# Optimization experiments

Hardware: AMD Instinct MI355X
Metric: run time of the kernel (lower is better)

Reference implementation:

```python
import jax, jax.numpy as jnp
import numpy as np

N, E, E_LBL = 50000, 800000, 200000
D_IN, H = 128, 128


def setup_inputs() -> dict:
    key = jax.random.key(0)
    ks = jax.random.split(key, 12)
    s = 0.05
    return {
        "x": jax.random.normal(ks[0], (N, D_IN), jnp.float32),
        "edge_index": jax.random.randint(ks[1], (2, E), 0, N, jnp.int64),
        "edge_label_index": jax.random.randint(ks[2], (2, E_LBL), 0, N, jnp.int64),
        "pre_w": jax.random.normal(ks[3], (D_IN, H), jnp.float32) * s,
        "pre_b": jax.random.normal(ks[4], (H,), jnp.float32) * s,
        "Wx": jax.random.normal(ks[5], (3, 2, H, H), jnp.float32) * s,  # gates z,r,h x cheb orders T0,T1
        "bx": jax.random.normal(ks[6], (3, H), jnp.float32) * s,
        "Wh": jax.random.normal(ks[7], (3, 2, H, H), jnp.float32) * s,
        "bh": jax.random.normal(ks[8], (3, H), jnp.float32) * s,
        "post_w": jax.random.normal(ks[9], (H, 2), jnp.float32) * s,
        "post_b": jax.random.normal(ks[10], (2,), jnp.float32) * s,
    }


def reference(x, edge_index, edge_label_index, pre_w, pre_b, Wx, bx, Wh, bh, post_w, post_b):
    n = x.shape[0]
    src, dst = edge_index[0], edge_index[1]

    # Scaled Chebyshev Laplacian (sym norm, lambda_max=2): L_hat = -D^{-1/2} A D^{-1/2}
    # (diagonal of L_hat is exactly 0, so only off-diagonal edge terms remain).
    deg = jax.ops.segment_sum(jnp.ones_like(src, dtype=x.dtype), src, num_segments=n)
    dinv = jnp.where(deg > 0, jax.lax.rsqrt(jnp.maximum(deg, 1.0)), 0.0)
    w = -(dinv[src] * dinv[dst])  # [E]

    def lap(v):  # L_hat @ v : gather src rows, weight, scatter-add at dst
        return jax.ops.segment_sum(w[:, None] * v[src], dst, num_segments=n)

    def cheb(v, Lv, W2, b):  # ChebConv K=2: T0(v)@W0 + T1(v)@W1 + b
        return v @ W2[0] + Lv @ W2[1] + b

    # pre: Linear(input_dim -> hidden)
    Xh = x @ pre_w + pre_b  # [N, H]
    LX = lap(Xh)

    # GConvGRU single step, H0 = 0
    Hc = jnp.zeros_like(Xh)
    LH = lap(Hc)
    Z = jax.nn.sigmoid(cheb(Xh, LX, Wx[0], bx[0]) + cheb(Hc, LH, Wh[0], bh[0]))
    R = jax.nn.sigmoid(cheb(Xh, LX, Wx[1], bx[1]) + cheb(Hc, LH, Wh[1], bh[1]))
    HR = Hc * R
    LHR = lap(HR)
    Ht = jnp.tanh(cheb(Xh, LX, Wx[2], bx[2]) + cheb(HR, LHR, Wh[2], bh[2]))
    Hc = Z * Hc + (1.0 - Z) * Ht

    h = jax.nn.relu(Hc)
    # link decoder: gather endpoints, hadamard, Linear(H->2), sum over logits
    hprod = h[edge_label_index[0]] * h[edge_label_index[1]]  # [E_lbl, H]
    out = hprod @ post_w + post_b  # [E_lbl, 2]
    return jnp.sum(out, axis=-1)  # [E_lbl]
```

## Files before the change

kernel.cpp:

```cpp
#include <hip/hip_runtime.h>
#include <math.h>


#define RND 4096
#define SORT_CAP 1536
#define CAPB 6144

typedef __attribute__((ext_vector_type(4))) float f32x4;
typedef __attribute__((ext_vector_type(8))) short short8;

static __device__ __forceinline__ unsigned short f2b(float f) {
  union { float f; unsigned u; } v; v.f = f;
  unsigned r = (v.u + 0x7fffu + ((v.u >> 16) & 1u)) >> 16;
  return (unsigned short)r;
}
static __device__ __forceinline__ float b2f(unsigned short s) {
  union { unsigned u; float f; } v; v.u = ((unsigned)s) << 16;
  return v.f;
}

__global__ __launch_bounds__(256) void prep_kernel(const float* __restrict__ pre_w, const float* __restrict__ Wx,
                                                   const float* __restrict__ bx, const float* __restrict__ bh,
                                                   const float* __restrict__ post_w, const float* __restrict__ post_b,
                                                   unsigned short* __restrict__ Bt1c, unsigned short* __restrict__ Btc2,
                                                   float* __restrict__ fb2, float* __restrict__ pwsum,
                                                   int* __restrict__ deg, int* __restrict__ binPos, int N) {
  int e = blockIdx.x * 256 + threadIdx.x;
  const int TOT = gridDim.x * 256;
  for (int i = e; i < N; i += TOT) deg[i] = 0;
  if (e < 256) binPos[e] = e * CAPB;
  if (e < 16384) {
    int kc = e >> 12, r = e & 4095, col = r >> 5, kk = r & 31;
    Bt1c[e] = f2b(pre_w[(kc * 32 + kk) * 128 + col]);
  }
  int e2 = e - 16384;
  if (e2 >= 0 && e2 < 65536) {
    int kc = e2 >> 13, r = e2 & 8191, cB = r >> 5, kk = r & 31;
    int k = kc * 32 + kk, half = k >> 7, ki = k & 127;
    int cb = cB >> 7, r7 = cB & 127, nw6 = r7 >> 6, u2 = r7 & 63;
    int g = (u2 >= 32) ? 2 : 0, hcol = cb * 64 + nw6 * 32 + (u2 & 31);
    Btc2[e2] = f2b(Wx[((g * 2 + half) * 128 + ki) * 128 + hcol]);
  }
  int e3 = e - (16384 + 65536);
  if (e3 >= 0 && e3 < 256) {
    int cB = e3;
    int cb = cB >> 7, r7 = cB & 127, nw6 = r7 >> 6, u2 = r7 & 63;
    int g = (u2 >= 32) ? 2 : 0, hcol = cb * 64 + nw6 * 32 + (u2 & 31);
    fb2[cB] = bx[g * 128 + hcol] + bh[g * 128 + hcol];
  }
  int e4 = e - (16384 + 65536 + 256);
  if (e4 >= 0 && e4 < 128) pwsum[e4] = post_w[2 * e4] + post_w[2 * e4 + 1];
  if (e4 == 128) pwsum[128] = post_b[0] + post_b[1];
}

union SMemU {
  struct { unsigned short As[128 * 40]; unsigned short Bs[128 * 40]; } g;
  struct { unsigned ent[RND]; int hist[256], scanbuf[256], lstart[256],
           lofs[256], gbase[256]; unsigned char ebin[RND]; } s;
};

__global__ __launch_bounds__(256) void mega1_kernel(const float* __restrict__ x,
                                                    const unsigned short* __restrict__ Bt1c,
                                                    const float* __restrict__ pre_b,
                                                    unsigned short* __restrict__ Xq,
                                                    const int* __restrict__ ei, int* __restrict__ binPos,
                                                    unsigned* __restrict__ bins, int* __restrict__ deg,
                                                    int N, int E, int RB) {
  __shared__ SMemU sm;
  const int t = threadIdx.x;

  if ((int)blockIdx.x < RB) {
    unsigned short* As = sm.g.As;
    unsigned short* Bs = sm.g.Bs;
    const int r0 = blockIdx.x * 128;
    const int w = t >> 6, lane = t & 63;
    const int m = lane & 15, q = lane >> 4;
    const int mw = (w >> 1) * 64, nw = (w & 1) * 64;

    f32x4 acc[4][4];
#pragma unroll
    for (int i = 0; i < 4; ++i)
#pragma unroll
      for (int j = 0; j < 4; ++j) acc[i][j] = {0.f, 0.f, 0.f, 0.f};

    const int arow = t >> 1, aseg = t & 1;
    const bool arow_ok = (r0 + arow) < N;
    const float* asrc0 = &x[(size_t)(r0 + arow) * 128 + aseg * 16];

    float4 cav[4]; short8 cbv0, cbv1;
    {
      if (arow_ok) {
#pragma unroll
        for (int i = 0; i < 4; ++i) cav[i] = *(const float4*)(asrc0 + i * 4);
      } else {
#pragma unroll
        for (int i = 0; i < 4; ++i) cav[i] = make_float4(0.f, 0.f, 0.f, 0.f);
      }
      const char* src = (const char*)Bt1c + t * 32;
      cbv0 = *(const short8*)src;
      cbv1 = *(const short8*)(src + 16);
    }

    for (int kc = 0; kc < 4; ++kc) {
      __syncthreads();
      {
        short8 t0, t1;
#pragma unroll
        for (int i = 0; i < 2; ++i) {
          t0[i * 4 + 0] = (short)f2b(cav[i].x); t0[i * 4 + 1] = (short)f2b(cav[i].y);
          t0[i * 4 + 2] = (short)f2b(cav[i].z); t0[i * 4 + 3] = (short)f2b(cav[i].w);
          t1[i * 4 + 0] = (short)f2b(cav[i + 2].x); t1[i * 4 + 1] = (short)f2b(cav[i + 2].y);
          t1[i * 4 + 2] = (short)f2b(cav[i + 2].z); t1[i * 4 + 3] = (short)f2b(cav[i + 2].w);
        }
        *(short8*)&As[arow * 40 + aseg * 16] = t0;
        *(short8*)&As[arow * 40 + aseg * 16 + 8] = t1;
        int bcol = t >> 1, boff = (t & 1) * 16;
        *(short8*)&Bs[bcol * 40 + boff] = cbv0;
        *(short8*)&Bs[bcol * 40 + boff + 8] = cbv1;
      }
      float4 nav[4]; short8 nbv0, nbv1;
      if (kc < 3) {
        if (arow_ok) {
          const float* src = asrc0 + (kc + 1) * 32;
#pragma unroll
          for (int i = 0; i < 4; ++i) nav[i] = *(const float4*)(src + i * 4);
        } else {
#pragma unroll
          for (int i = 0; i < 4; ++i) nav[i] = make_float4(0.f, 0.f, 0.f, 0.f);
        }
        const char* src = (const char*)Bt1c + (size_t)(kc + 1) * 8192 + t * 32;
        nbv0 = *(const short8*)src;
        nbv1 = *(const short8*)(src + 16);
      }
      __syncthreads();
      short8 af[4], bf[4];
#pragma unroll
      for (int i = 0; i < 4; ++i) af[i] = *(const short8*)&As[(mw + i * 16 + m) * 40 + q * 8];
#pragma unroll
      for (int j = 0; j < 4; ++j) bf[j] = *(const short8*)&Bs[(nw + j * 16 + m) * 40 + q * 8];
#pragma unroll
      for (int i = 0; i < 4; ++i)
#pragma unroll
        for (int j = 0; j < 4; ++j)
          acc[i][j] = __builtin_amdgcn_mfma_f32_16x16x32_bf16(af[i], bf[j], acc[i][j], 0, 0, 0);
      if (kc < 3) {
#pragma unroll
        for (int i = 0; i < 4; ++i) cav[i] = nav[i];
        cbv0 = nbv0; cbv1 = nbv1;
      }
    }

#pragma unroll
    for (int i = 0; i < 4; ++i) {
      int rb2 = r0 + mw + i * 16 + q * 4;
#pragma unroll
      for (int j = 0; j < 4; ++j) {
        int col = nw + j * 16 + m;
        float bias = pre_b[col];
#pragma unroll
        for (int r = 0; r < 4; ++r) {
          int row = rb2 + r;
          if (row < N) Xq[(size_t)row * 128 + col] = f2b(acc[i][j][r] + bias);
        }
      }
    }
    return;
  }

  unsigned* ent = sm.s.ent;
  unsigned char* ebin = sm.s.ebin;
  int* hist = sm.s.hist;
  int* scanbuf = sm.s.scanbuf;
  int* lstart = sm.s.lstart;
  int* lofs = sm.s.lofs;
  int* gbase = sm.s.gbase;
  const int sbid = (int)blockIdx.x - RB;
  const int snum = (int)gridDim.x - RB;
  for (long long base = (long long)sbid * RND; base < E; base += (long long)snum * RND) {
    int cnt = (int)(((long long)E - base < RND) ? (E - base) : RND);
    if (t < 256) hist[t] = 0;
    __syncthreads();
    unsigned my_e[16]; int my_b[16];
#pragma unroll
    for (int u = 0; u < 16; ++u) {
      int i = u * 256 + t;
      my_b[u] = -1;
      if (i < cnt) {
        int idx = (int)base + i;
        int s = ei[idx], d = ei[E + idx];
        atomicAdd(&deg[s], 1);
        my_b[u] = d >> 8;
        my_e[u] = (unsigned)s | ((unsigned)(d & 255) << 16);
        atomicAdd(&hist[my_b[u]], 1);
      }
    }
    __syncthreads();
    scanbuf[t] = hist[t];
    __syncthreads();
    for (int d = 1; d < 256; d <<= 1) {
      int v = (t >= d) ? scanbuf[t - d] : 0;
      __syncthreads();
      scanbuf[t] += v;
      __syncthreads();
    }
    int excl = scanbuf[t] - hist[t];
    lstart[t] = excl;
    lofs[t] = excl;
    if (hist[t] > 0) gbase[t] = atomicAdd(&binPos[t], hist[t]);
    __syncthreads();
#pragma unroll
    for (int u = 0; u < 16; ++u) {
      if (my_b[u] >= 0) {
        int p = atomicAdd(&lofs[my_b[u]], 1);
        ent[p] = my_e[u];
        ebin[p] = (unsigned char)my_b[u];
      }
    }
    __syncthreads();
    for (int i = t; i < cnt; i += 256) {
      int b = ebin[i];
      int pos = gbase[b] + (i - lstart[b]);
      if (pos < (b + 1) * CAPB) bins[pos] = ent[i];
    }
    __syncthreads();
  }
}

__global__ __launch_bounds__(512) void lap_bin_kernel(const unsigned short* __restrict__ Xq,
                                                      unsigned short* __restrict__ LXc,
                                                      const unsigned* __restrict__ bins,
                                                      const int* __restrict__ binPos,
                                                      const int* __restrict__ deg, int N) {
  __shared__ unsigned short sortS[SORT_CAP];
  __shared__ float sortW[SORT_CAP];
  __shared__ int hist[64], start[64], scanbuf[64], off[64];
  const int t = threadIdx.x;
  const int bin = blockIdx.x >> 2, qt = blockIdx.x & 3;
  const int lo = bin * CAPB;
  int T = binPos[bin] - lo;
  if (T > CAPB) T = CAPB;
  const unsigned* __restrict__ ebase = &bins[lo];
  if (t < 64) hist[t] = 0;
  __syncthreads();
  for (int i = t; i < T; i += 512) {
    unsigned e = ebase[i];
    int dl = (e >> 16) & 255;
    if ((dl >> 6) == qt) atomicAdd(&hist[dl & 63], 1);
  }
  __syncthreads();
  if (t < 64) scanbuf[t] = hist[t];
  __syncthreads();
  for (int d = 1; d < 64; d <<= 1) {
    int v = (t < 64 && t >= d) ? scanbuf[t - d] : 0;
    __syncthreads();
    if (t < 64) scanbuf[t] += v;
    __syncthreads();
  }
  if (t < 64) { int s0 = scanbuf[t] - hist[t]; start[t] = s0; off[t] = s0; }
  __syncthreads();
  for (int i = t; i < T; i += 512) {
    unsigned e = ebase[i];
    int dl = (e >> 16) & 255;
    if ((dl >> 6) == qt) {
      int s = (int)(e & 0xFFFFu);
      int p = atomicAdd(&off[dl & 63], 1);
      if (p < SORT_CAP) {
        int dg = deg[s];
        sortS[p] = (unsigned short)s;
        sortW[p] = dg > 0 ? rsqrtf((float)dg) : 0.0f;
      }
    }
  }
  __syncthreads();
  const int wv = t >> 6, lane = t & 63;
  for (int n = wv; n < 64; n += 8) {
    int node = bin * 256 + qt * 64 + n;
    if (node >= N) break;
    int st = start[n], cnum = hist[n];
    float ax = 0.f, ay = 0.f;
    for (int j = 0; j < cnum; j += 8) {
      unsigned v[8]; float ws[8];
#pragma unroll
      for (int u = 0; u < 8; ++u) {
        int idx = j + u;
        int s = 0; float w = 0.f;
        if (idx < cnum) { s = sortS[st + idx]; w = sortW[st + idx]; }
        ws[u] = w;
        v[u] = *(const unsigned*)((const char*)Xq + (size_t)s * 256 + lane * 4);
      }
#pragma unroll
      for (int u = 0; u < 8; ++u) {
        union { unsigned u32; float f; } fl, fh;
        fl.u32 = v[u] << 16; fh.u32 = v[u] & 0xffff0000u;
        ax += ws[u] * fl.f;
        ay += ws[u] * fh.f;
      }
    }
    int dgn = deg[node];
    float wd = dgn > 0 ? -rsqrtf((float)dgn) : 0.0f;
    unsigned o = (unsigned)f2b(ax * wd) | ((unsigned)f2b(ay * wd) << 16);
    *(unsigned*)((char*)LXc + (size_t)node * 256 + lane * 4) = o;
  }
}

__global__ __launch_bounds__(256) void gemm2_mfma(const unsigned short* __restrict__ Xq,
                                                  const unsigned short* __restrict__ LXc,
                                                  const unsigned short* __restrict__ Btc2,
                                                  const float* __restrict__ fb2,
                                                  unsigned short* __restrict__ hb, int N) {
  __shared__ unsigned short As[128 * 40];
  __shared__ unsigned short Bs[128 * 40];
  const int t = threadIdx.x;
  const int rb = blockIdx.x >> 1, cb = blockIdx.x & 1;
  const int r0 = rb * 128;
  const int w = t >> 6, lane = t & 63;
  const int m = lane & 15, q = lane >> 4;
  const int mw = (w >> 1) * 64, nw = (w & 1) * 64;

  f32x4 acc[4][4];
#pragma unroll
  for (int i = 0; i < 4; ++i)
#pragma unroll
    for (int j = 0; j < 4; ++j) acc[i][j] = {0.f, 0.f, 0.f, 0.f};

  const int arow = t >> 1;
  const int aoff = (t & 1) * 32;
  const char* aXq = (const char*)Xq + (size_t)(r0 + arow) * 256 + aoff;
  const char* aLX = (const char*)LXc + (size_t)(r0 + arow) * 256 + aoff;
  const char* bsrc0 = (const char*)Btc2 + (size_t)cb * 8192 + t * 32;

  short8 cav0, cav1, cbv0, cbv1;
  cav0 = *(const short8*)aXq;
  cav1 = *(const short8*)(aXq + 16);
  cbv0 = *(const short8*)bsrc0;
  cbv1 = *(const short8*)(bsrc0 + 16);

  for (int kc = 0; kc < 8; ++kc) {
    __syncthreads();
    *(short8*)&As[arow * 40 + (aoff >> 1)] = cav0;
    *(short8*)&As[arow * 40 + (aoff >> 1) + 8] = cav1;
    {
      int bcol = t >> 1, boff = (t & 1) * 16;
      *(short8*)&Bs[bcol * 40 + boff] = cbv0;
      *(short8*)&Bs[bcol * 40 + boff + 8] = cbv1;
    }
    short8 nav0, nav1, nbv0, nbv1;
    if (kc < 7) {
      int kn = kc + 1;
      const char* asrc = (kn < 4) ? (aXq + kn * 64) : (aLX + (kn - 4) * 64);
      nav0 = *(const short8*)asrc;
      nav1 = *(const short8*)(asrc + 16);
      const char* bsrc = bsrc0 + (size_t)kn * 16384;
      nbv0 = *(const short8*)bsrc;
      nbv1 = *(const short8*)(bsrc + 16);
    }
    __syncthreads();
    short8 af[4], bf[4];
#pragma unroll
    for (int i = 0; i < 4; ++i) af[i] = *(const short8*)&As[(mw + i * 16 + m) * 40 + q * 8];
#pragma unroll
    for (int j = 0; j < 4; ++j) bf[j] = *(const short8*)&Bs[(nw + j * 16 + m) * 40 + q * 8];
#pragma unroll
    for (int i = 0; i < 4; ++i)
#pragma unroll
      for (int j = 0; j < 4; ++j)
        acc[i][j] = __builtin_amdgcn_mfma_f32_16x16x32_bf16(af[i], bf[j], acc[i][j], 0, 0, 0);
    if (kc < 7) { cav0 = nav0; cav1 = nav1; cbv0 = nbv0; cbv1 = nbv1; }
  }

#pragma unroll
  for (int i = 0; i < 4; ++i) {
    int rbase = r0 + mw + i * 16 + q * 4;
#pragma unroll
    for (int jz = 0; jz < 2; ++jz) {
      int cBz = cb * 128 + nw + jz * 16 + m;
      int hc = cb * 64 + (nw >> 1) + jz * 16 + m;
      float bz = fb2[cBz], bt = fb2[cBz + 32];
#pragma unroll
      for (int r = 0; r < 4; ++r) {
        int row = rbase + r;
        if (row < N) {
          float zp = acc[i][jz][r] + bz;
          float tp = acc[i][jz + 2][r] + bt;
          float zs = 1.0f / (1.0f + __expf(-zp));
          float th = tanhf(tp);
          hb[(size_t)row * 128 + hc] = f2b(fmaxf((1.0f - zs) * th, 0.0f));
        }
      }
    }
  }
}

__global__ __launch_bounds__(256) void decoder_kernel(const unsigned short* __restrict__ hb,
                                                      const int* __restrict__ eli,
                                                      const float* __restrict__ pwsum, float* __restrict__ out, int M) {
  int t = threadIdx.x;
  int i = blockIdx.x * 16 + (t >> 4);
  int l = t & 15;
  if (i >= M) return;
  int a = eli[i], b = eli[M + i];
  int k = l * 8;
  short8 va = *(const short8*)&hb[(size_t)a * 128 + k];
  short8 vb = *(const short8*)&hb[(size_t)b * 128 + k];
  const float4* pwp = (const float4*)&pwsum[k];
  float4 p0 = pwp[0], p1 = pwp[1];
  float s = 0.0f;
  s += b2f((unsigned short)va[0]) * b2f((unsigned short)vb[0]) * p0.x;
  s += b2f((unsigned short)va[1]) * b2f((unsigned short)vb[1]) * p0.y;
  s += b2f((unsigned short)va[2]) * b2f((unsigned short)vb[2]) * p0.z;
  s += b2f((unsigned short)va[3]) * b2f((unsigned short)vb[3]) * p0.w;
  s += b2f((unsigned short)va[4]) * b2f((unsigned short)vb[4]) * p1.x;
  s += b2f((unsigned short)va[5]) * b2f((unsigned short)vb[5]) * p1.y;
  s += b2f((unsigned short)va[6]) * b2f((unsigned short)vb[6]) * p1.z;
  s += b2f((unsigned short)va[7]) * b2f((unsigned short)vb[7]) * p1.w;
#pragma unroll
  for (int off = 8; off; off >>= 1) s += __shfl_xor(s, off);
  if (l == 0) out[i] = s + pwsum[128];
}

extern "C" void kernel_launch(void* const* d_in, const int* in_sizes, int n_in,
                              void* d_out, int out_size, void* d_ws, size_t ws_size,
                              hipStream_t stream) {
  const float* x      = (const float*)d_in[0];
  const int*   ei     = (const int*)d_in[1];
  const int*   eli    = (const int*)d_in[2];
  const float* pre_w  = (const float*)d_in[3];
  const float* pre_b  = (const float*)d_in[4];
  const float* Wx     = (const float*)d_in[5];
  const float* bx     = (const float*)d_in[6];
  const float* bh     = (const float*)d_in[8];
  const float* post_w = (const float*)d_in[9];
  const float* post_b = (const float*)d_in[10];
  float* out = (float*)d_out;

  const int N = in_sizes[0] / 128;
  const int E = in_sizes[1] / 2;
  const int M = in_sizes[2] / 2;
  const int RB = (N + 127) / 128;
  const int NBIN = (N + 255) / 256;
  const int SCAT = (E + RND - 1) / RND;

  char* W = (char*)d_ws;
  size_t o = 0;
  int* deg = (int*)(W + o);       o += (size_t)N * 4;
  int* binPos = (int*)(W + o);    o += 1024;
  o = (o + 255) & ~(size_t)255;
  unsigned* bins = (unsigned*)(W + o); o += (size_t)NBIN * CAPB * 4;
  o = (o + 255) & ~(size_t)255;
  unsigned short* Xq = (unsigned short*)(W + o);  o += (size_t)RB * 128 * 256;
  unsigned short* LXc = (unsigned short*)(W + o); o += (size_t)RB * 128 * 256;
  unsigned short* hb = (unsigned short*)(W + o);  o += (size_t)N * 256;
  unsigned short* Bt1c = (unsigned short*)(W + o); o += 32768;
  unsigned short* Btc2 = (unsigned short*)(W + o); o += 131072;
  float* fb2 = (float*)(W + o);  o += 1024;
  float* pwsum = (float*)(W + o); o += 768;

  prep_kernel<<<322, 256, 0, stream>>>(pre_w, Wx, bx, bh, post_w, post_b, Bt1c, Btc2, fb2, pwsum,
                                       deg, binPos, N);
  mega1_kernel<<<RB + SCAT, 256, 0, stream>>>(x, Bt1c, pre_b, Xq, ei, binPos, bins, deg, N, E, RB);
  lap_bin_kernel<<<NBIN * 4, 512, 0, stream>>>(Xq, LXc, bins, binPos, deg, N);
  gemm2_mfma<<<RB * 2, 256, 0, stream>>>(Xq, LXc, Btc2, fb2, hb, N);
  decoder_kernel<<<(M + 15) / 16, 256, 0, stream>>>(hb, eli, pwsum, out, M);
}
```

Baseline: 213.4 us.

## Scatter edges directly to global bins, drop block prefix scan and LDS staging

The binning path of mega1_kernel no longer runs a 256-entry prefix scan or stages entries in shared memory before writing them to global bins. Each thread now takes its slot with a shared atomic on a per-bin counter and writes straight to the global bin position. The round size is halved and the per-thread edge count drops from 16 to 8, which cuts registers and removes several barriers per round. In exchange, global writes within a bin are no longer contiguous and coalesced, and there are more rounds, each with its own global atomic reservation per bin.

```diff
diff --git a/kernel.cpp b/kernel.cpp
--- a/kernel.cpp
+++ b/kernel.cpp
@@ -2,7 +2,8 @@
 #include <math.h>
 
 
-#define RND 4096
+#define RND 2048
+#define EPT 8
 #define SORT_CAP 1536
 #define CAPB 6144
 
@@ -55,8 +56,7 @@
 
 union SMemU {
   struct { unsigned short As[128 * 40]; unsigned short Bs[128 * 40]; } g;
-  struct { unsigned ent[RND]; int hist[256], scanbuf[256], lstart[256],
-           lofs[256], gbase[256]; unsigned char ebin[RND]; } s;
+  struct { int hist[256], lofs[256], gbase[256]; } s;
 };
 
 __global__ __launch_bounds__(256) void mega1_kernel(const float* __restrict__ x,
@@ -167,22 +167,18 @@
     return;
   }
 
-  unsigned* ent = sm.s.ent;
-  unsigned char* ebin = sm.s.ebin;
   int* hist = sm.s.hist;
-  int* scanbuf = sm.s.scanbuf;
-  int* lstart = sm.s.lstart;
   int* lofs = sm.s.lofs;
   int* gbase = sm.s.gbase;
   const int sbid = (int)blockIdx.x - RB;
   const int snum = (int)gridDim.x - RB;
   for (long long base = (long long)sbid * RND; base < E; base += (long long)snum * RND) {
     int cnt = (int)(((long long)E - base < RND) ? (E - base) : RND);
-    if (t < 256) hist[t] = 0;
-    __syncthreads();
-    unsigned my_e[16]; int my_b[16];
-#pragma unroll
-    for (int u = 0; u < 16; ++u) {
+    if (t < 256) { hist[t] = 0; lofs[t] = 0; }
+    __syncthreads();
+    unsigned my_e[EPT]; int my_b[EPT];
+#pragma unroll
+    for (int u = 0; u < EPT; ++u) {
       int i = u * 256 + t;
       my_b[u] = -1;
       if (i < cnt) {
@@ -195,32 +191,16 @@
       }
     }
     __syncthreads();
-    scanbuf[t] = hist[t];
-    __syncthreads();
-    for (int d = 1; d < 256; d <<= 1) {
-      int v = (t >= d) ? scanbuf[t - d] : 0;
-      __syncthreads();
-      scanbuf[t] += v;
-      __syncthreads();
-    }
-    int excl = scanbuf[t] - hist[t];
-    lstart[t] = excl;
-    lofs[t] = excl;
-    if (hist[t] > 0) gbase[t] = atomicAdd(&binPos[t], hist[t]);
-    __syncthreads();
-#pragma unroll
-    for (int u = 0; u < 16; ++u) {
+    if (t < 256 && hist[t] > 0) gbase[t] = atomicAdd(&binPos[t], hist[t]);
+    __syncthreads();
+#pragma unroll
+    for (int u = 0; u < EPT; ++u) {
       if (my_b[u] >= 0) {
-        int p = atomicAdd(&lofs[my_b[u]], 1);
-        ent[p] = my_e[u];
-        ebin[p] = (unsigned char)my_b[u];
-      }
-    }
-    __syncthreads();
-    for (int i = t; i < cnt; i += 256) {
-      int b = ebin[i];
-      int pos = gbase[b] + (i - lstart[b]);
-      if (pos < (b + 1) * CAPB) bins[pos] = ent[i];
+        int b = my_b[u];
+        int p = atomicAdd(&lofs[b], 1);
+        int pos = gbase[b] + p;
+        if (pos < (b + 1) * CAPB) bins[pos] = my_e[u];
+      }
     }
     __syncthreads();
   }
```

After: 215.6 us. About the same (+1.0%).

## Fuse Laplacian aggregation with gate GEMM, keeping LX tile in shared memory

Applied to the files above, without the earlier changes.

Merges the binned Laplacian kernel and the MFMA gate GEMM into one kernel. Each 64-node block stages its Xq rows into padded shared memory, writes the aggregated LX rows next to them, then runs the K=256 GEMM from LDS with B fragments loaded straight from global memory. The gate weight layout in prep is reordered so each wave owns 16 hidden columns for both the z and h gates. This removes the LXc round trip through global memory and one launch, but the GEMM now runs on 64-row tiles, uses more LDS per block, and reloads B from global/L2 in every block.

```diff
diff --git a/kernel.cpp b/kernel.cpp
--- a/kernel.cpp
+++ b/kernel.cpp
@@ -5,6 +5,7 @@
 #define RND 4096
 #define SORT_CAP 1536
 #define CAPB 6144
+#define APAD 260
 
 typedef __attribute__((ext_vector_type(4))) float f32x4;
 typedef __attribute__((ext_vector_type(8))) short short8;
@@ -37,15 +38,15 @@
   if (e2 >= 0 && e2 < 65536) {
     int kc = e2 >> 13, r = e2 & 8191, cB = r >> 5, kk = r & 31;
     int k = kc * 32 + kk, half = k >> 7, ki = k & 127;
-    int cb = cB >> 7, r7 = cB & 127, nw6 = r7 >> 6, u2 = r7 & 63;
-    int g = (u2 >= 32) ? 2 : 0, hcol = cb * 64 + nw6 * 32 + (u2 & 31);
+    int s5 = cB >> 5, r5 = cB & 31, jz = r5 >> 4, m = r5 & 15;
+    int g = jz ? 2 : 0, hcol = s5 * 16 + m;
     Btc2[e2] = f2b(Wx[((g * 2 + half) * 128 + ki) * 128 + hcol]);
   }
   int e3 = e - (16384 + 65536);
   if (e3 >= 0 && e3 < 256) {
     int cB = e3;
-    int cb = cB >> 7, r7 = cB & 127, nw6 = r7 >> 6, u2 = r7 & 63;
-    int g = (u2 >= 32) ? 2 : 0, hcol = cb * 64 + nw6 * 32 + (u2 & 31);
+    int s5 = cB >> 5, r5 = cB & 31, jz = r5 >> 4, m = r5 & 15;
+    int g = jz ? 2 : 0, hcol = s5 * 16 + m;
     fb2[cB] = bx[g * 128 + hcol] + bh[g * 128 + hcol];
   }
   int e4 = e - (16384 + 65536 + 256);
@@ -226,16 +227,29 @@
   }
 }
 
-__global__ __launch_bounds__(512) void lap_bin_kernel(const unsigned short* __restrict__ Xq,
-                                                      unsigned short* __restrict__ LXc,
-                                                      const unsigned* __restrict__ bins,
-                                                      const int* __restrict__ binPos,
-                                                      const int* __restrict__ deg, int N) {
+__global__ __launch_bounds__(512) void lap_gemm2_kernel(const unsigned short* __restrict__ Xq,
+                                                        const unsigned* __restrict__ bins,
+                                                        const int* __restrict__ binPos,
+                                                        const int* __restrict__ deg,
+                                                        const unsigned short* __restrict__ Btc2,
+                                                        const float* __restrict__ fb2,
+                                                        unsigned short* __restrict__ hb, int N) {
+  __shared__ unsigned short As[64 * APAD];
   __shared__ unsigned short sortS[SORT_CAP];
   __shared__ float sortW[SORT_CAP];
   __shared__ int hist[64], start[64], scanbuf[64], off[64];
   const int t = threadIdx.x;
   const int bin = blockIdx.x >> 2, qt = blockIdx.x & 3;
+  const int node0 = bin * 256 + qt * 64;
+
+  {
+    int row = t >> 3, seg = t & 7;
+    const char* src = (const char*)Xq + (size_t)(node0 + row) * 256 + seg * 32;
+    short8 v0 = *(const short8*)src;
+    short8 v1 = *(const short8*)(src + 16);
+    *(short8*)&As[row * APAD + seg * 16] = v0;
+    *(short8*)&As[row * APAD + seg * 16 + 8] = v1;
+  }
   const int lo = bin * CAPB;
   int T = binPos[bin] - lo;
   if (T > CAPB) T = CAPB;
@@ -272,10 +286,9 @@
     }
   }
   __syncthreads();
+
   const int wv = t >> 6, lane = t & 63;
   for (int n = wv; n < 64; n += 8) {
-    int node = bin * 256 + qt * 64 + n;
-    if (node >= N) break;
     int st = start[n], cnum = hist[n];
     float ax = 0.f, ay = 0.f;
     for (int j = 0; j < cnum; j += 8) {
@@ -296,96 +309,47 @@
         ay += ws[u] * fh.f;
       }
     }
-    int dgn = deg[node];
+    int nd = node0 + n;
+    int dgn = (nd < N) ? deg[nd] : 0;
     float wd = dgn > 0 ? -rsqrtf((float)dgn) : 0.0f;
     unsigned o = (unsigned)f2b(ax * wd) | ((unsigned)f2b(ay * wd) << 16);
-    *(unsigned*)((char*)LXc + (size_t)node * 256 + lane * 4) = o;
-  }
-}
-
-__global__ __launch_bounds__(256) void gemm2_mfma(const unsigned short* __restrict__ Xq,
-                                                  const unsigned short* __restrict__ LXc,
-                                                  const unsigned short* __restrict__ Btc2,
-                                                  const float* __restrict__ fb2,
-                                                  unsigned short* __restrict__ hb, int N) {
-  __shared__ unsigned short As[128 * 40];
-  __shared__ unsigned short Bs[128 * 40];
-  const int t = threadIdx.x;
-  const int rb = blockIdx.x >> 1, cb = blockIdx.x & 1;
-  const int r0 = rb * 128;
-  const int w = t >> 6, lane = t & 63;
+    *(unsigned*)((char*)As + (size_t)n * (APAD * 2) + 256 + lane * 4) = o;
+  }
+  __syncthreads();
+
   const int m = lane & 15, q = lane >> 4;
-  const int mw = (w >> 1) * 64, nw = (w & 1) * 64;
-
-  f32x4 acc[4][4];
-#pragma unroll
-  for (int i = 0; i < 4; ++i)
-#pragma unroll
-    for (int j = 0; j < 4; ++j) acc[i][j] = {0.f, 0.f, 0.f, 0.f};
-
-  const int arow = t >> 1;
-  const int aoff = (t & 1) * 32;
-  const char* aXq = (const char*)Xq + (size_t)(r0 + arow) * 256 + aoff;
-  const char* aLX = (const char*)LXc + (size_t)(r0 + arow) * 256 + aoff;
-  const char* bsrc0 = (const char*)Btc2 + (size_t)cb * 8192 + t * 32;
-
-  short8 cav0, cav1, cbv0, cbv1;
-  cav0 = *(const short8*)aXq;
-  cav1 = *(const short8*)(aXq + 16);
-  cbv0 = *(const short8*)bsrc0;
-  cbv1 = *(const short8*)(bsrc0 + 16);
-
+  f32x4 acc[4][2];
+#pragma unroll
+  for (int i = 0; i < 4; ++i) { acc[i][0] = {0.f, 0.f, 0.f, 0.f}; acc[i][1] = {0.f, 0.f, 0.f, 0.f}; }
+  const char* b0 = (const char*)Btc2 + (size_t)(wv * 32 + m) * 64 + q * 16;
+  const char* b1 = (const char*)Btc2 + (size_t)(wv * 32 + 16 + m) * 64 + q * 16;
+#pragma unroll 2
   for (int kc = 0; kc < 8; ++kc) {
-    __syncthreads();
-    *(short8*)&As[arow * 40 + (aoff >> 1)] = cav0;
-    *(short8*)&As[arow * 40 + (aoff >> 1) + 8] = cav1;
-    {
-      int bcol = t >> 1, boff = (t & 1) * 16;
-      *(short8*)&Bs[bcol * 40 + boff] = cbv0;
-      *(short8*)&Bs[bcol * 40 + boff + 8] = cbv1;
-    }
-    short8 nav0, nav1, nbv0, nbv1;
-    if (kc < 7) {
-      int kn = kc + 1;
-      const char* asrc = (kn < 4) ? (aXq + kn * 64) : (aLX + (kn - 4) * 64);
-      nav0 = *(const short8*)asrc;
-      nav1 = *(const short8*)(asrc + 16);
-      const char* bsrc = bsrc0 + (size_t)kn * 16384;
-      nbv0 = *(const short8*)bsrc;
-      nbv1 = *(const short8*)(bsrc + 16);
-    }
-    __syncthreads();
-    short8 af[4], bf[4];
-#pragma unroll
-    for (int i = 0; i < 4; ++i) af[i] = *(const short8*)&As[(mw + i * 16 + m) * 40 + q * 8];
-#pragma unroll
-    for (int j = 0; j < 4; ++j) bf[j] = *(const short8*)&Bs[(nw + j * 16 + m) * 40 + q * 8];
+    short8 bf0 = *(const short8*)(b0 + (size_t)kc * 16384);
+    short8 bf1 = *(const short8*)(b1 + (size_t)kc * 16384);
+    short8 af[4];
 #pragma unroll
     for (int i = 0; i < 4; ++i)
-#pragma unroll
-      for (int j = 0; j < 4; ++j)
-        acc[i][j] = __builtin_amdgcn_mfma_f32_16x16x32_bf16(af[i], bf[j], acc[i][j], 0, 0, 0);
-    if (kc < 7) { cav0 = nav0; cav1 = nav1; cbv0 = nbv0; cbv1 = nbv1; }
-  }
-
+      af[i] = *(const short8*)&As[(i * 16 + m) * APAD + kc * 32 + q * 8];
+#pragma unroll
+    for (int i = 0; i < 4; ++i) {
+      acc[i][0] = __builtin_amdgcn_mfma_f32_16x16x32_bf16(af[i], bf0, acc[i][0], 0, 0, 0);
+      acc[i][1] = __builtin_amdgcn_mfma_f32_16x16x32_bf16(af[i], bf1, acc[i][1], 0, 0, 0);
+    }
+  }
+
+  float bz = fb2[wv * 32 + m], bt = fb2[wv * 32 + 16 + m];
 #pragma unroll
   for (int i = 0; i < 4; ++i) {
-    int rbase = r0 + mw + i * 16 + q * 4;
-#pragma unroll
-    for (int jz = 0; jz < 2; ++jz) {
-      int cBz = cb * 128 + nw + jz * 16 + m;
-      int hc = cb * 64 + (nw >> 1) + jz * 16 + m;
-      float bz = fb2[cBz], bt = fb2[cBz + 32];
-#pragma unroll
-      for (int r = 0; r < 4; ++r) {
-        int row = rbase + r;
-        if (row < N) {
-          float zp = acc[i][jz][r] + bz;
-          float tp = acc[i][jz + 2][r] + bt;
-          float zs = 1.0f / (1.0f + __expf(-zp));
-          float th = tanhf(tp);
-          hb[(size_t)row * 128 + hc] = f2b(fmaxf((1.0f - zs) * th, 0.0f));
-        }
+#pragma unroll
+    for (int r = 0; r < 4; ++r) {
+      int row = node0 + i * 16 + q * 4 + r;
+      if (row < N) {
+        float zp = acc[i][0][r] + bz;
+        float tp = acc[i][1][r] + bt;
+        float zs = 1.0f / (1.0f + __expf(-zp));
+        float th = tanhf(tp);
+        hb[(size_t)row * 128 + wv * 16 + m] = f2b(fmaxf((1.0f - zs) * th, 0.0f));
       }
     }
   }
@@ -439,6 +403,7 @@
   const int RB = (N + 127) / 128;
   const int NBIN = (N + 255) / 256;
   const int SCAT = (E + RND - 1) / RND;
+  const size_t XQROWS = (size_t)NBIN * 256;
 
   char* W = (char*)d_ws;
   size_t o = 0;
@@ -447,8 +412,7 @@
   o = (o + 255) & ~(size_t)255;
   unsigned* bins = (unsigned*)(W + o); o += (size_t)NBIN * CAPB * 4;
   o = (o + 255) & ~(size_t)255;
-  unsigned short* Xq = (unsigned short*)(W + o);  o += (size_t)RB * 128 * 256;
-  unsigned short* LXc = (unsigned short*)(W + o); o += (size_t)RB * 128 * 256;
+  unsigned short* Xq = (unsigned short*)(W + o);  o += XQROWS * 256;
   unsigned short* hb = (unsigned short*)(W + o);  o += (size_t)N * 256;
   unsigned short* Bt1c = (unsigned short*)(W + o); o += 32768;
   unsigned short* Btc2 = (unsigned short*)(W + o); o += 131072;
@@ -458,7 +422,6 @@
   prep_kernel<<<322, 256, 0, stream>>>(pre_w, Wx, bx, bh, post_w, post_b, Bt1c, Btc2, fb2, pwsum,
                                        deg, binPos, N);
   mega1_kernel<<<RB + SCAT, 256, 0, stream>>>(x, Bt1c, pre_b, Xq, ei, binPos, bins, deg, N, E, RB);
-  lap_bin_kernel<<<NBIN * 4, 512, 0, stream>>>(Xq, LXc, bins, binPos, deg, N);
-  gemm2_mfma<<<RB * 2, 256, 0, stream>>>(Xq, LXc, Btc2, fb2, hb, N);
+  lap_gemm2_kernel<<<NBIN * 4, 512, 0, stream>>>(Xq, bins, binPos, deg, Btc2, fb2, hb, N);
   decoder_kernel<<<(M + 15) / 16, 256, 0, stream>>>(hb, eli, pwsum, out, M);
 }
```

After: 218.5 us. +2.4%, slower.
